# Kernel optimization log

Hardware: AMD Instinct MI355X
Metric: run time of the kernel (lower is better)

The kernel has to match this reference:

```python
import jax, jax.numpy as jnp
import numpy as np
from jax import lax

ITERATIONS = 10
B, I, D, J, E = 512, 7, 512, 64, 128


def setup_inputs() -> dict:
    key = jax.random.key(0)
    k1, k2, k3 = jax.random.split(key, 3)
    f_bid = jax.random.normal(k1, (B, I, D), dtype=jnp.float32)
    p_bi = jax.random.uniform(k2, (B, I), dtype=jnp.float32)
    weights = jax.random.normal(k3, (I, D, J, E), dtype=jnp.float32)
    return {"f_bid": f_bid, "p_bi": p_bi, "weights": weights}


def reference(f_bid, p_bi, weights):
    # Precompute the per-capsule vote tensor once: [B, I, J, E]
    f_W_bije = jnp.einsum('bid,idje->bije', f_bid, weights)
    b = f_bid.shape[0]
    j, e = weights.shape[2], weights.shape[3]
    c0 = jnp.ones((b, j, e), dtype=f_bid.dtype)

    def body(c_bj, _):
        # routing logits over output capsules j, softmax over j (dim=-1 of 'bij')
        r_bij = jax.nn.softmax(jnp.einsum('bije,bje->bij', f_W_bije, c_bj), axis=-1)
        c_next = jnp.einsum('bi,bij,bije->bje', p_bi, r_bij, f_W_bije)
        return c_next, r_bij

    c_bj, r_stack = lax.scan(body, c0, None, length=ITERATIONS)
    return c_bj, r_stack[-1]
```

## Files before the change

kernel.cpp:

```cpp
#include <hip/hip_runtime.h>
#include <hip/hip_bf16.h>

#define B_SZ 512
#define I_SZ 7
#define D_SZ 512
#define J_SZ 64
#define E_SZ 128
#define N_SZ 8192
#define ITERS 10

typedef __attribute__((ext_vector_type(8))) short bf16x8;
typedef __attribute__((ext_vector_type(4))) float f32x4;

#if defined(__has_builtin)
#if __has_builtin(__builtin_amdgcn_cvt_pk_bf16_f32)
#define HAVE_CVT_PK_BF16 1
#endif
#endif

__device__ inline void split2(float x0, float x1, unsigned& hp, unsigned& lp) {
#ifdef HAVE_CVT_PK_BF16
    auto h = __builtin_amdgcn_cvt_pk_bf16_f32(x0, x1);
    hp = __builtin_bit_cast(unsigned, h);
    union { unsigned u; float f; } b0, b1;
    b0.u = hp << 16;
    b1.u = hp & 0xFFFF0000u;
    auto l = __builtin_amdgcn_cvt_pk_bf16_f32(x0 - b0.f, x1 - b1.f);
    lp = __builtin_bit_cast(unsigned, l);
#else
    union { float f; unsigned u; } u0, u1;
    u0.f = x0; u1.f = x1;
    unsigned r0 = u0.u + 0x7FFF + ((u0.u >> 16) & 1);
    unsigned r1 = u1.u + 0x7FFF + ((u1.u >> 16) & 1);
    hp = __builtin_amdgcn_perm(r1, r0, 0x07060302);
    union { unsigned u; float f; } h0, h1;
    h0.u = r0 & 0xFFFF0000u;
    h1.u = r1 & 0xFFFF0000u;
    union { float f; unsigned u; } s0, s1;
    s0.f = x0 - h0.f; s1.f = x1 - h1.f;
    unsigned q0 = s0.u + 0x7FFF + ((s0.u >> 16) & 1);
    unsigned q1 = s1.u + 0x7FFF + ((s1.u >> 16) & 1);
    lp = __builtin_amdgcn_perm(q1, q0, 0x07060302);
#endif
}

__global__ __launch_bounds__(512, 2) void vote_gemm_mfma(
    const float* __restrict__ f,
    const float* __restrict__ W,
    float* __restrict__ fW)
{
    const int i  = blockIdx.z;
    const int m0 = blockIdx.y * 256;
    const int n0 = blockIdx.x * 256;
    const int th = threadIdx.x;
    const int lane = th & 63;
    const int wave = th >> 6;
    const int wr   = wave >> 2;
    const int wc   = wave & 3;
    const int quad = lane >> 4;
    const int lm   = lane & 15;

    __shared__ short Ah_s[2][256 * 32];
    __shared__ short Al_s[2][256 * 32];
    __shared__ short Bh_s[2][256 * 32];
    __shared__ short Bl_s[2][256 * 32];

    const int sm = th >> 1;
    const int kh = th & 1;
    const int swz = (sm >> 1) & 3;
    const int wo0 = sm * 32 + (((kh << 1) | 0) ^ swz) * 8;
    const int wo1 = sm * 32 + (((kh << 1) | 1) ^ swz) * 8;

    const float* aPtr = f + (size_t)(m0 + sm) * (I_SZ * D_SZ) + (size_t)i * D_SZ + kh * 16;
    const float* bPtr = W + (size_t)i * D_SZ * N_SZ + (size_t)(kh * 16) * N_SZ + n0 + sm;

    const int fpos8 = (quad ^ ((lm >> 1) & 3)) * 8;

    f32x4 acc[8][4];
#pragma unroll
    for (int a = 0; a < 8; ++a)
#pragma unroll
        for (int c = 0; c < 4; ++c)
            acc[a][c] = (f32x4){0.f, 0.f, 0.f, 0.f};

    float av[16], bv[16];
    auto stage_load = [&](int kt) {
        const float* pa = aPtr + kt * 32;
        float4 t0 = *(const float4*)(pa);
        float4 t1 = *(const float4*)(pa + 4);
        float4 t2 = *(const float4*)(pa + 8);
        float4 t3 = *(const float4*)(pa + 12);
        av[0]=t0.x;  av[1]=t0.y;  av[2]=t0.z;  av[3]=t0.w;
        av[4]=t1.x;  av[5]=t1.y;  av[6]=t1.z;  av[7]=t1.w;
        av[8]=t2.x;  av[9]=t2.y;  av[10]=t2.z; av[11]=t2.w;
        av[12]=t3.x; av[13]=t3.y; av[14]=t3.z; av[15]=t3.w;
        const float* pb = bPtr + (size_t)kt * 32 * N_SZ;
#pragma unroll
        for (int r = 0; r < 16; ++r) bv[r] = pb[(size_t)r * N_SZ];
    };
    auto stage_write = [&](int slot) {
        short* qAh = &Ah_s[slot][0]; short* qAl = &Al_s[slot][0];
        short* qBh = &Bh_s[slot][0]; short* qBl = &Bl_s[slot][0];
        uint4 h, l;
        split2(av[0],  av[1],  h.x, l.x); split2(av[2],  av[3],  h.y, l.y);
        split2(av[4],  av[5],  h.z, l.z); split2(av[6],  av[7],  h.w, l.w);
        *(uint4*)&qAh[wo0] = h; *(uint4*)&qAl[wo0] = l;
        split2(av[8],  av[9],  h.x, l.x); split2(av[10], av[11], h.y, l.y);
        split2(av[12], av[13], h.z, l.z); split2(av[14], av[15], h.w, l.w);
        *(uint4*)&qAh[wo1] = h; *(uint4*)&qAl[wo1] = l;
        split2(bv[0],  bv[1],  h.x, l.x); split2(bv[2],  bv[3],  h.y, l.y);
        split2(bv[4],  bv[5],  h.z, l.z); split2(bv[6],  bv[7],  h.w, l.w);
        *(uint4*)&qBh[wo0] = h; *(uint4*)&qBl[wo0] = l;
        split2(bv[8],  bv[9],  h.x, l.x); split2(bv[10], bv[11], h.y, l.y);
        split2(bv[12], bv[13], h.z, l.z); split2(bv[14], bv[15], h.w, l.w);
        *(uint4*)&qBh[wo1] = h; *(uint4*)&qBl[wo1] = l;
    };

    stage_load(0);
    stage_write(0);
    __syncthreads();

    for (int t = 0; t < 16; ++t) {
        const int s = t & 1;
        const short* pAh = &Ah_s[s][0]; const short* pAl = &Al_s[s][0];
        const short* pBh = &Bh_s[s][0]; const short* pBl = &Bl_s[s][0];

        if (t < 15) stage_load(t + 1);
        __builtin_amdgcn_sched_barrier(0);

        bf16x8 Bf_h[4], Bf_l[4];
#pragma unroll
        for (int ns = 0; ns < 4; ++ns) {
            const int o = (wc * 64 + ns * 16 + lm) * 32 + fpos8;
            Bf_h[ns] = *(const bf16x8*)&pBh[o];
            Bf_l[ns] = *(const bf16x8*)&pBl[o];
        }

#pragma unroll
        for (int ph = 0; ph < 4; ++ph) {
            bf16x8 Af_h[2], Af_l[2];
#pragma unroll
            for (int u = 0; u < 2; ++u) {
                const int ms = ph * 2 + u;
                const int o = (wr * 128 + ms * 16 + lm) * 32 + fpos8;
                Af_h[u] = *(const bf16x8*)&pAh[o];
                Af_l[u] = *(const bf16x8*)&pAl[o];
            }
            __builtin_amdgcn_s_setprio(1);
#pragma unroll
            for (int u = 0; u < 2; ++u) {
                const int ms = ph * 2 + u;
#pragma unroll
                for (int ns = 0; ns < 4; ++ns) {
                    acc[ms][ns] = __builtin_amdgcn_mfma_f32_16x16x32_bf16(Af_h[u], Bf_h[ns], acc[ms][ns], 0, 0, 0);
                    acc[ms][ns] = __builtin_amdgcn_mfma_f32_16x16x32_bf16(Af_h[u], Bf_l[ns], acc[ms][ns], 0, 0, 0);
                    acc[ms][ns] = __builtin_amdgcn_mfma_f32_16x16x32_bf16(Af_l[u], Bf_h[ns], acc[ms][ns], 0, 0, 0);
                }
            }
            __builtin_amdgcn_s_setprio(0);
            if (ph < 3) __builtin_amdgcn_s_barrier();
        }

        __builtin_amdgcn_sched_barrier(0);
        if (t < 15) stage_write(s ^ 1);
        __syncthreads();
    }

#pragma unroll
    for (int ms = 0; ms < 8; ++ms) {
        const int rowb = m0 + wr * 128 + ms * 16 + quad * 4;
#pragma unroll
        for (int ns = 0; ns < 4; ++ns) {
            const int col = n0 + wc * 64 + ns * 16 + lm;
#pragma unroll
            for (int r = 0; r < 4; ++r)
                fW[((size_t)(rowb + r) * I_SZ + i) * N_SZ + col] = acc[ms][ns][r];
        }
    }
}

__global__ __launch_bounds__(1024) void routing_kernel(
    const float* __restrict__ fW,
    const float* __restrict__ p,
    float* __restrict__ c_out,
    float* __restrict__ r_out)
{
    const int b   = blockIdx.x;
    const int tid = threadIdx.x;
    const int j   = tid >> 4;
    const int sub = tid & 15;

    __shared__ float G_sh[64][49];
    __shared__ float s_sh[64][9];
    __shared__ float w_sh[2][64][9];
    __shared__ float p_sh[8];

    if (tid < I_SZ) p_sh[tid] = p[(size_t)b * I_SZ + tid];

    float4 fw[I_SZ][2];
    const float* base = fW + (size_t)b * I_SZ * N_SZ + j * E_SZ + sub * 8;
#pragma unroll
    for (int i = 0; i < I_SZ; ++i) {
        fw[i][0] = *(const float4*)(base + (size_t)i * N_SZ);
        fw[i][1] = *(const float4*)(base + (size_t)i * N_SZ + 4);
    }

#pragma unroll
    for (int i = 0; i < I_SZ; ++i) {
        float s = fw[i][0].x + fw[i][0].y + fw[i][0].z + fw[i][0].w
                + fw[i][1].x + fw[i][1].y + fw[i][1].z + fw[i][1].w;
        s += __shfl_xor(s, 1); s += __shfl_xor(s, 2);
        s += __shfl_xor(s, 4); s += __shfl_xor(s, 8);
        if (sub == 0) s_sh[j][i] = s;
#pragma unroll
        for (int i2 = i; i2 < I_SZ; ++i2) {
            float g = fw[i][0].x * fw[i2][0].x + fw[i][0].y * fw[i2][0].y
                    + fw[i][0].z * fw[i2][0].z + fw[i][0].w * fw[i2][0].w
                    + fw[i][1].x * fw[i2][1].x + fw[i][1].y * fw[i2][1].y
                    + fw[i][1].z * fw[i2][1].z + fw[i][1].w * fw[i2][1].w;
            g += __shfl_xor(g, 1); g += __shfl_xor(g, 2);
            g += __shfl_xor(g, 4); g += __shfl_xor(g, 8);
            if (sub == 0) { G_sh[j][i * 7 + i2] = g; G_sh[j][i2 * 7 + i] = g; }
        }
    }
    __syncthreads();

    for (int t = 0; t < ITERS; ++t) {
        if (tid < I_SZ * 64) {
            const int ii = tid >> 6;
            const int jj = tid & 63;
            float l;
            if (t == 0) {
                l = s_sh[jj][ii];
            } else {
                const int rb = t & 1;
                l = 0.f;
#pragma unroll
                for (int i2 = 0; i2 < I_SZ; ++i2)
                    l = fmaf(w_sh[rb][jj][i2], G_sh[jj][ii * 7 + i2], l);
            }
            float mx = l;
#pragma unroll
            for (int off = 32; off > 0; off >>= 1)
                mx = fmaxf(mx, __shfl_xor(mx, off));
            float ex = __expf(l - mx);
            float sm = ex;
#pragma unroll
            for (int off = 32; off > 0; off >>= 1)
                sm += __shfl_xor(sm, off);
            float r = ex / sm;
            if (t == ITERS - 1)
                r_out[(size_t)b * (I_SZ * J_SZ) + ii * 64 + jj] = r;
            w_sh[(t + 1) & 1][jj][ii] = p_sh[ii] * r;
        }
        __syncthreads();
    }

    float4 a0 = make_float4(0.f, 0.f, 0.f, 0.f);
    float4 a1 = make_float4(0.f, 0.f, 0.f, 0.f);
#pragma unroll
    for (int i = 0; i < I_SZ; ++i) {
        float wv = w_sh[ITERS & 1][j][i];
        a0.x = fmaf(wv, fw[i][0].x, a0.x); a0.y = fmaf(wv, fw[i][0].y, a0.y);
        a0.z = fmaf(wv, fw[i][0].z, a0.z); a0.w = fmaf(wv, fw[i][0].w, a0.w);
        a1.x = fmaf(wv, fw[i][1].x, a1.x); a1.y = fmaf(wv, fw[i][1].y, a1.y);
        a1.z = fmaf(wv, fw[i][1].z, a1.z); a1.w = fmaf(wv, fw[i][1].w, a1.w);
    }
    float* dst = c_out + (size_t)b * N_SZ + j * E_SZ + sub * 8;
    *(float4*)(dst)     = a0;
    *(float4*)(dst + 4) = a1;
}

extern "C" void kernel_launch(void* const* d_in, const int* in_sizes, int n_in,
                              void* d_out, int out_size, void* d_ws, size_t ws_size,
                              hipStream_t stream) {
    const float* f = (const float*)d_in[0];
    const float* p = (const float*)d_in[1];
    const float* W = (const float*)d_in[2];
    float* out = (float*)d_out;
    float* fW  = (float*)d_ws;

    vote_gemm_mfma<<<dim3(N_SZ / 256, B_SZ / 256, I_SZ), 512, 0, stream>>>(f, W, fW);
    routing_kernel<<<B_SZ, 1024, 0, stream>>>(fW, p, out, out + (size_t)B_SZ * N_SZ);
}
```

Measured before the change: 323.8 us.

## Stage W tiles into LDS via direct global-to-LDS DMA as fp32

The B operand (weights) is now copied straight from global memory into a swizzled fp32 LDS buffer with global_load_lds, and the per-tile register staging of W is dropped. The bf16 hi/lo split for B moves to after the LDS read, so each wave splits its own fragments instead of splitting once during the store. This is meant to remove the strided scalar global loads of W (16 per thread per tile) and the register pressure they cause. The intra-tile s_barrier phases are also removed. In exchange, the B conversion work is repeated by every wave, and strided fp32 LDS reads may cause bank conflicts.

```diff
diff --git a/kernel.cpp b/kernel.cpp
--- a/kernel.cpp
+++ b/kernel.cpp
@@ -44,6 +44,12 @@
 #endif
 }
 
+__device__ inline void gload16(const float* g, float* l) {
+    __builtin_amdgcn_global_load_lds(
+        (const __attribute__((address_space(1))) void*)g,
+        (__attribute__((address_space(3))) void*)l, 16, 0, 0);
+}
+
 __global__ __launch_bounds__(512, 2) void vote_gemm_mfma(
     const float* __restrict__ f,
     const float* __restrict__ W,
@@ -62,17 +68,24 @@
 
     __shared__ short Ah_s[2][256 * 32];
     __shared__ short Al_s[2][256 * 32];
-    __shared__ short Bh_s[2][256 * 32];
-    __shared__ short Bl_s[2][256 * 32];
+    __shared__ float B_s [2][32 * 256];
 
     const int sm = th >> 1;
     const int kh = th & 1;
     const int swz = (sm >> 1) & 3;
     const int wo0 = sm * 32 + (((kh << 1) | 0) ^ swz) * 8;
     const int wo1 = sm * 32 + (((kh << 1) | 1) ^ swz) * 8;
-
     const float* aPtr = f + (size_t)(m0 + sm) * (I_SZ * D_SZ) + (size_t)i * D_SZ + kh * 16;
-    const float* bPtr = W + (size_t)i * D_SZ * N_SZ + (size_t)(kh * 16) * N_SZ + n0 + sm;
+
+    const float* bSrc[4];
+#pragma unroll
+    for (int ci = 0; ci < 4; ++ci) {
+        const int idx = ci * 512 + th;
+        const int kB  = idx >> 6;
+        const int cB  = idx & 63;
+        const int c   = cB ^ (((kB >> 3) & 3) << 1);
+        bSrc[ci] = W + (size_t)i * D_SZ * N_SZ + (size_t)kB * N_SZ + n0 + (c << 2);
+    }
 
     const int fpos8 = (quad ^ ((lm >> 1) & 3)) * 8;
 
@@ -83,8 +96,8 @@
         for (int c = 0; c < 4; ++c)
             acc[a][c] = (f32x4){0.f, 0.f, 0.f, 0.f};
 
-    float av[16], bv[16];
-    auto stage_load = [&](int kt) {
+    float av[16];
+    auto stageA_load = [&](int kt) {
         const float* pa = aPtr + kt * 32;
         float4 t0 = *(const float4*)(pa);
         float4 t1 = *(const float4*)(pa + 4);
@@ -94,13 +107,14 @@
         av[4]=t1.x;  av[5]=t1.y;  av[6]=t1.z;  av[7]=t1.w;
         av[8]=t2.x;  av[9]=t2.y;  av[10]=t2.z; av[11]=t2.w;
         av[12]=t3.x; av[13]=t3.y; av[14]=t3.z; av[15]=t3.w;
-        const float* pb = bPtr + (size_t)kt * 32 * N_SZ;
-#pragma unroll
-        for (int r = 0; r < 16; ++r) bv[r] = pb[(size_t)r * N_SZ];
     };
-    auto stage_write = [&](int slot) {
+    auto stageB_dma = [&](int kt, int slot) {
+#pragma unroll
+        for (int ci = 0; ci < 4; ++ci)
+            gload16(bSrc[ci] + (size_t)kt * 32 * N_SZ, &B_s[slot][(ci * 512 + th) * 4]);
+    };
+    auto stageA_write = [&](int slot) {
         short* qAh = &Ah_s[slot][0]; short* qAl = &Al_s[slot][0];
-        short* qBh = &Bh_s[slot][0]; short* qBl = &Bl_s[slot][0];
         uint4 h, l;
         split2(av[0],  av[1],  h.x, l.x); split2(av[2],  av[3],  h.y, l.y);
         split2(av[4],  av[5],  h.z, l.z); split2(av[6],  av[7],  h.w, l.w);
@@ -108,61 +122,60 @@
         split2(av[8],  av[9],  h.x, l.x); split2(av[10], av[11], h.y, l.y);
         split2(av[12], av[13], h.z, l.z); split2(av[14], av[15], h.w, l.w);
         *(uint4*)&qAh[wo1] = h; *(uint4*)&qAl[wo1] = l;
-        split2(bv[0],  bv[1],  h.x, l.x); split2(bv[2],  bv[3],  h.y, l.y);
-        split2(bv[4],  bv[5],  h.z, l.z); split2(bv[6],  bv[7],  h.w, l.w);
-        *(uint4*)&qBh[wo0] = h; *(uint4*)&qBl[wo0] = l;
-        split2(bv[8],  bv[9],  h.x, l.x); split2(bv[10], bv[11], h.y, l.y);
-        split2(bv[12], bv[13], h.z, l.z); split2(bv[14], bv[15], h.w, l.w);
-        *(uint4*)&qBh[wo1] = h; *(uint4*)&qBl[wo1] = l;
     };
 
-    stage_load(0);
-    stage_write(0);
+    stageA_load(0);
+    stageA_write(0);
+    stageB_dma(0, 0);
+    asm volatile("s_waitcnt vmcnt(0)" ::: "memory");
     __syncthreads();
 
     for (int t = 0; t < 16; ++t) {
         const int s = t & 1;
         const short* pAh = &Ah_s[s][0]; const short* pAl = &Al_s[s][0];
-        const short* pBh = &Bh_s[s][0]; const short* pBl = &Bl_s[s][0];
-
-        if (t < 15) stage_load(t + 1);
+        const float* Bb  = &B_s[s][0];
+
+        if (t < 15) {
+            stageA_load(t + 1);
+            stageB_dma(t + 1, s ^ 1);
+        }
         __builtin_amdgcn_sched_barrier(0);
 
         bf16x8 Bf_h[4], Bf_l[4];
 #pragma unroll
         for (int ns = 0; ns < 4; ++ns) {
-            const int o = (wc * 64 + ns * 16 + lm) * 32 + fpos8;
-            Bf_h[ns] = *(const bf16x8*)&pBh[o];
-            Bf_l[ns] = *(const bf16x8*)&pBl[o];
-        }
-
-#pragma unroll
-        for (int ph = 0; ph < 4; ++ph) {
-            bf16x8 Af_h[2], Af_l[2];
-#pragma unroll
-            for (int u = 0; u < 2; ++u) {
-                const int ms = ph * 2 + u;
-                const int o = (wr * 128 + ms * 16 + lm) * 32 + fpos8;
-                Af_h[u] = *(const bf16x8*)&pAh[o];
-                Af_l[u] = *(const bf16x8*)&pAl[o];
-            }
+            const int nloc = wc * 64 + ns * 16 + lm;
+            const float* bp = Bb + quad * (8 * 256)
+                            + ((((nloc >> 2) ^ (quad << 1))) << 2) + (nloc & 3);
+            const float b0 = bp[0*256], b1 = bp[1*256], b2 = bp[2*256], b3 = bp[3*256];
+            const float b4 = bp[4*256], b5 = bp[5*256], b6 = bp[6*256], b7 = bp[7*256];
+            uint4 h, l;
+            split2(b0, b1, h.x, l.x);
+            split2(b2, b3, h.y, l.y);
+            split2(b4, b5, h.z, l.z);
+            split2(b6, b7, h.w, l.w);
+            Bf_h[ns] = __builtin_bit_cast(bf16x8, h);
+            Bf_l[ns] = __builtin_bit_cast(bf16x8, l);
+        }
+
+#pragma unroll
+        for (int ms = 0; ms < 8; ++ms) {
+            const int o = (wr * 128 + ms * 16 + lm) * 32 + fpos8;
+            const bf16x8 Af_h = *(const bf16x8*)&pAh[o];
+            const bf16x8 Af_l = *(const bf16x8*)&pAl[o];
             __builtin_amdgcn_s_setprio(1);
 #pragma unroll
-            for (int u = 0; u < 2; ++u) {
-                const int ms = ph * 2 + u;
-#pragma unroll
-                for (int ns = 0; ns < 4; ++ns) {
-                    acc[ms][ns] = __builtin_amdgcn_mfma_f32_16x16x32_bf16(Af_h[u], Bf_h[ns], acc[ms][ns], 0, 0, 0);
-                    acc[ms][ns] = __builtin_amdgcn_mfma_f32_16x16x32_bf16(Af_h[u], Bf_l[ns], acc[ms][ns], 0, 0, 0);
-                    acc[ms][ns] = __builtin_amdgcn_mfma_f32_16x16x32_bf16(Af_l[u], Bf_h[ns], acc[ms][ns], 0, 0, 0);
-                }
+            for (int ns = 0; ns < 4; ++ns) {
+                acc[ms][ns] = __builtin_amdgcn_mfma_f32_16x16x32_bf16(Af_h, Bf_h[ns], acc[ms][ns], 0, 0, 0);
+                acc[ms][ns] = __builtin_amdgcn_mfma_f32_16x16x32_bf16(Af_h, Bf_l[ns], acc[ms][ns], 0, 0, 0);
+                acc[ms][ns] = __builtin_amdgcn_mfma_f32_16x16x32_bf16(Af_l, Bf_h[ns], acc[ms][ns], 0, 0, 0);
             }
             __builtin_amdgcn_s_setprio(0);
-            if (ph < 3) __builtin_amdgcn_s_barrier();
-        }
-
+        }
         __builtin_amdgcn_sched_barrier(0);
-        if (t < 15) stage_write(s ^ 1);
+
+        if (t < 15) stageA_write(s ^ 1);
+        asm volatile("s_waitcnt vmcnt(0)" ::: "memory");
         __syncthreads();
     }
 
```

Result: no change. 327.7 us (+1.2%).
